# Kernel optimization log

Hardware: AMD Instinct MI355X
Metric: run time of the kernel (lower is better)

The kernel has to match this reference:

```python
import jax, jax.numpy as jnp
import numpy as np

B, QT, KT = 4, 1024, 1024
Q_SIZE, K_SIZE, EMB, HEADS = 1024, 1024, 1024, 8
HEAD_DIM = EMB // HEADS


def setup_inputs() -> dict:
    key = jax.random.key(0)
    ks = jax.random.split(key, 8)
    query = jax.random.normal(ks[0], (B, QT, Q_SIZE), dtype=jnp.float32)
    key_t = jax.random.normal(ks[1], (B, KT, K_SIZE), dtype=jnp.float32)
    mask = jax.random.randint(ks[2], (B, QT, KT), 0, 2, dtype=jnp.int32)
    # Linear weights stored as (in, out); torch Linear computes x @ W.T, equivalent here.
    sq = 1.0 / np.sqrt(Q_SIZE)
    sk = 1.0 / np.sqrt(K_SIZE)
    se = 1.0 / np.sqrt(EMB)
    Wq = jax.random.uniform(ks[3], (Q_SIZE, EMB), jnp.float32, -sq, sq)
    Wk = jax.random.uniform(ks[4], (K_SIZE, EMB), jnp.float32, -sk, sk)
    Wv = jax.random.uniform(ks[5], (K_SIZE, EMB), jnp.float32, -sk, sk)
    Wu = jax.random.uniform(ks[6], (EMB, EMB), jnp.float32, -se, se)
    bu = jax.random.uniform(ks[7], (EMB,), jnp.float32, -se, se)
    return {"query": query, "key": key_t, "mask": mask,
            "Wq": Wq, "Wk": Wk, "Wv": Wv, "Wu": Wu, "bu": bu}


def reference(query, key, mask, Wq, Wk, Wv, Wu, bu):
    b, q_t, _ = query.shape
    k_t = key.shape[1]
    q = (query @ Wq).reshape(b, q_t, HEADS, HEAD_DIM)   # b i n d
    k = (key @ Wk).reshape(b, k_t, HEADS, HEAD_DIM)     # b j n d
    v = (key @ Wv).reshape(b, k_t, HEADS, HEAD_DIM)
    # NOTE: original module defines self.scale but never applies it.
    att_score = jnp.einsum('bind,bjnd->bijn', q, k)
    att_score = jnp.where(mask[..., None] == 0, jnp.float32(-1e9), att_score)
    att_prob = jax.nn.softmax(att_score, axis=2)        # softmax over key axis j
    att_vec = jnp.einsum('bijn,bjnd->bind', att_prob, v).reshape(b, q_t, EMB)
    return att_vec @ Wu + bu
```

## Files before the change

### kernel.cpp

```cpp
#include <hip/hip_runtime.h>
#include <hip/hip_bf16.h>


typedef __attribute__((ext_vector_type(8))) short bf16x8;
typedef __attribute__((ext_vector_type(4))) float f32x4;

static constexpr int BB = 4;
static constexpr int TT = 1024;
static constexpr int EE = 1024;
static constexpr int HH = 8;
static constexpr int DD = 128;

static __device__ __forceinline__ unsigned short f2b(float x) {
  union { float f; unsigned int u; } c; c.f = x;
  unsigned int r = c.u + 0x7fffu + ((c.u >> 16) & 1u);
  return (unsigned short)(r >> 16);
}

static __device__ __forceinline__ unsigned int cvtpk(float lo, float hi) {
  unsigned int r;
  asm("v_cvt_pk_bf16_f32 %0, %1, %2" : "=v"(r) : "v"(lo), "v"(hi));
  return r;
}

static __device__ __forceinline__ float exp2x(float x) {
  float r;
  asm("v_exp_f32 %0, %1" : "=v"(r) : "v"(x));
  return r;
}

static __device__ __forceinline__ void gload_lds16(const void* g, void* l) {
  __builtin_amdgcn_global_load_lds(
      (const __attribute__((address_space(1))) unsigned int*)g,
      (__attribute__((address_space(3))) unsigned int*)l, 16, 0, 0);
}

__global__ __launch_bounds__(256) void cvt_kernel(
    const float* __restrict__ qf, const float* __restrict__ kf,
    unsigned short* __restrict__ qb, unsigned short* __restrict__ kb) {
  int i = blockIdx.x * 256 + threadIdx.x;
  float4 a = ((const float4*)qf)[i];
  ushort4 oa; oa.x = f2b(a.x); oa.y = f2b(a.y); oa.z = f2b(a.z); oa.w = f2b(a.w);
  ((ushort4*)qb)[i] = oa;
  float4 b = ((const float4*)kf)[i];
  ushort4 ob; ob.x = f2b(b.x); ob.y = f2b(b.y); ob.z = f2b(b.z); ob.w = f2b(b.w);
  ((ushort4*)kb)[i] = ob;
}

struct WT4 { const float* src[4]; unsigned short* dst[4]; float scale[4]; };

__global__ __launch_bounds__(256) void wtrans_kernel(WT4 wt) {
  const float* src = wt.src[blockIdx.z];
  unsigned short* dst = wt.dst[blockIdx.z];
  const float sc = wt.scale[blockIdx.z];
  __shared__ float tile[32][33];
  int n0 = blockIdx.x * 32, k0 = blockIdx.y * 32;
  int tx = threadIdx.x, ty = threadIdx.y;
#pragma unroll
  for (int i = 0; i < 4; ++i)
    tile[ty + i * 8][tx] = src[(size_t)(k0 + ty + i * 8) * EE + n0 + tx];
  __syncthreads();
#pragma unroll
  for (int i = 0; i < 4; ++i)
    dst[(size_t)(n0 + ty + i * 8) * EE + k0 + tx] = f2b(tile[tx][ty + i * 8] * sc);
}

__global__ __launch_bounds__(256) void vtrans_kernel(
    const unsigned short* __restrict__ vp, unsigned short* __restrict__ vt) {
  int bh = blockIdx.z; int b = bh >> 3, h = bh & 7;
  int d0 = blockIdx.x * 32, kt0 = blockIdx.y * 32;
  __shared__ unsigned short tile[32][33];
  int tx = threadIdx.x, ty = threadIdx.y;
#pragma unroll
  for (int i = 0; i < 4; ++i)
    tile[ty + i * 8][tx] =
        vp[(size_t)(b * TT + kt0 + ty + i * 8) * EE + h * DD + d0 + tx];
  __syncthreads();
#pragma unroll
  for (int i = 0; i < 4; ++i)
    vt[(size_t)((b * HH + h) * DD + d0 + ty + i * 8) * TT + kt0 + tx] =
        tile[tx][ty + i * 8];
}

__global__ __launch_bounds__(256) void maskpack_kernel(
    const int* __restrict__ mask, unsigned long long* __restrict__ mbits) {
  int row = blockIdx.x * 4 + (threadIdx.x >> 6);
  int lane = threadIdx.x & 63;
  const int* mrow = mask + (size_t)row * TT;
  unsigned long long myw = 0;
#pragma unroll
  for (int jw = 0; jw < 16; ++jw) {
    unsigned long long bal = __ballot(mrow[jw * 64 + lane] != 0);
    if (lane == jw) myw = bal;
  }
  if (lane < 16) mbits[(size_t)row * 16 + lane] = myw;
}

static __device__ __forceinline__ void gemm_core(
    const unsigned short* __restrict__ A, const unsigned short* __restrict__ Bt,
    unsigned short* __restrict__ Cb) {
  constexpr int K = EE, N = EE;
  __shared__ __align__(16) unsigned short As[128 * 64];
  __shared__ __align__(16) unsigned short Bs[128 * 64];
  const int tid = threadIdx.x, lane = tid & 63, w = tid >> 6;
  const int wm = w >> 1, wn = w & 1;
  const int bm = blockIdx.x, bn = blockIdx.y;
  const int g4 = lane >> 4, l15 = lane & 15;

  f32x4 acc[4][4] = {};

  for (int kt = 0; kt < K / 64; ++kt) {
    const int k0 = kt * 64;
#pragma unroll
    for (int it = 0; it < 4; ++it) {
      int idx = it * 256 + tid;
      int r = idx >> 3, c = (idx & 7) ^ (r & 7);
      gload_lds16(A + (size_t)(bm * 128 + r) * K + k0 + c * 8, As + idx * 8);
      gload_lds16(Bt + (size_t)(bn * 128 + r) * K + k0 + c * 8, Bs + idx * 8);
    }
    __syncthreads();
    bf16x8 af[2][4], bf[2][4];
#pragma unroll
    for (int kc2 = 0; kc2 < 2; ++kc2) {
      int co = ((kc2 * 4 + g4) ^ (l15 & 7)) * 8;
#pragma unroll
      for (int i = 0; i < 4; ++i) {
        af[kc2][i] = *(const bf16x8*)(As + (wm * 64 + i * 16 + l15) * 64 + co);
        bf[kc2][i] = *(const bf16x8*)(Bs + (wn * 64 + i * 16 + l15) * 64 + co);
      }
    }
#pragma unroll
    for (int kc2 = 0; kc2 < 2; ++kc2)
#pragma unroll
      for (int i = 0; i < 4; ++i)
#pragma unroll
        for (int j = 0; j < 4; ++j)
          acc[i][j] = __builtin_amdgcn_mfma_f32_16x16x32_bf16(
              af[kc2][i], bf[kc2][j], acc[i][j], 0, 0, 0);
    __syncthreads();
  }

  const int rr = g4 * 4;
#pragma unroll
  for (int i = 0; i < 4; ++i)
#pragma unroll
    for (int j = 0; j < 4; ++j) {
      int row = bm * 128 + wm * 64 + i * 16 + rr;
      int col = bn * 128 + wn * 64 + j * 16 + l15;
#pragma unroll
      for (int r = 0; r < 4; ++r)
        Cb[(size_t)(row + r) * N + col] = f2b(acc[i][j][r]);
    }
}

struct Gemm3 { const unsigned short* A[3]; const unsigned short* Bt[3];
               unsigned short* C[3]; };

__global__ __launch_bounds__(256) void proj_gemm_kernel(Gemm3 g) {
  int z = blockIdx.z;
  gemm_core(g.A[z], g.Bt[z], g.C[z]);
}

__global__ __launch_bounds__(256) void out_gemm_kernel(
    const unsigned short* __restrict__ A, const unsigned short* __restrict__ Bt,
    float* __restrict__ Cf, const float* __restrict__ bias) {
  constexpr int K = EE, N = EE;
  __shared__ __align__(16) unsigned short As[64 * 32];
  __shared__ __align__(16) unsigned short Bs[128 * 32];
  const int tid = threadIdx.x, lane = tid & 63, w = tid >> 6;
  const int wm = w >> 1, wn = w & 1;
  const int bm = blockIdx.x, bn = blockIdx.y;
  const int g4 = lane >> 4, l15 = lane & 15;

  f32x4 acc[2][4] = {};

  for (int kt = 0; kt < K / 32; ++kt) {
    const int k0 = kt * 32;
    {
      int row = tid >> 2, c = tid & 3;
      gload_lds16(A + (size_t)(bm * 64 + row) * K + k0 + c * 8, As + tid * 8);
    }
#pragma unroll
    for (int it = 0; it < 2; ++it) {
      int idx = it * 256 + tid;
      int row = idx >> 2, c = idx & 3;
      gload_lds16(Bt + (size_t)(bn * 128 + row) * K + k0 + c * 8, Bs + idx * 8);
    }
    __syncthreads();
    bf16x8 af[2], bf[4];
#pragma unroll
    for (int i = 0; i < 2; ++i)
      af[i] = *(const bf16x8*)(As + (wm * 32 + i * 16 + l15) * 32 + g4 * 8);
#pragma unroll
    for (int j = 0; j < 4; ++j)
      bf[j] = *(const bf16x8*)(Bs + (wn * 64 + j * 16 + l15) * 32 + g4 * 8);
#pragma unroll
    for (int i = 0; i < 2; ++i)
#pragma unroll
      for (int j = 0; j < 4; ++j)
        acc[i][j] = __builtin_amdgcn_mfma_f32_16x16x32_bf16(af[i], bf[j],
                                                            acc[i][j], 0, 0, 0);
    __syncthreads();
  }

  const int rr = g4 * 4;
#pragma unroll
  for (int i = 0; i < 2; ++i)
#pragma unroll
    for (int j = 0; j < 4; ++j) {
      int row = bm * 64 + wm * 32 + i * 16 + rr;
      int col = bn * 128 + wn * 64 + j * 16 + l15;
#pragma unroll
      for (int r = 0; r < 4; ++r)
        Cf[(size_t)(row + r) * N + col] = acc[i][j][r] + bias[col];
    }
}

__global__ __launch_bounds__(512, 4) void attn_kernel(
    const unsigned short* __restrict__ q, const unsigned short* __restrict__ k,
    const unsigned short* __restrict__ vt,
    const unsigned long long* __restrict__ mbits,
    unsigned short* __restrict__ av) {
  extern __shared__ __align__(16) char smem[];

  const int tid = threadIdx.x, lane = tid & 63, w = tid >> 6;
  const int grp = w >> 2, qw = w & 3;
  const int orig = blockIdx.x + 16 * blockIdx.y + 128 * blockIdx.z;
  const int qt = (orig >> 3) & 15;
  const int pair = ((orig & 7) << 2) | (orig >> 7);
  const int h = pair & 7, b = pair >> 3;
  const int i0 = qt * 64 + qw * 16;
  const int g4 = lane >> 4, l15 = lane & 15;
  const int swz = (l15 & 7) << 4;

  bf16x8 aq[4];
  {
    const unsigned short* qb =
        q + (size_t)(b * TT + i0 + l15) * EE + h * DD + g4 * 8;
#pragma unroll
    for (int kc = 0; kc < 4; ++kc) aq[kc] = *(const bf16x8*)(qb + kc * 32);
  }

  const unsigned short* sptr[4];
  int ldsb[4];
  size_t sadv;
  if (w < 4) {
    int kg = w >> 1, kh = w & 1;
    const unsigned short* kb0 = k + (size_t)(b * TT) * EE + h * DD;
#pragma unroll
    for (int p = 0; p < 4; ++p) {
      int idx = kh * 256 + p * 64 + lane;
      int kr = idx >> 4, c = (idx & 15) ^ (kr & 7);
      sptr[p] = kb0 + (size_t)(kg * 512 + kr) * EE + c * 8;
      ldsb[p] = kg * 8192 + (kh * 256 + p * 64) * 16;
    }
    sadv = (size_t)32 * EE;
  } else {
    int vw = w - 4;
    const unsigned short* vb0 = vt + (size_t)((b * HH + h) * DD) * TT;
#pragma unroll
    for (int p = 0; p < 4; ++p) {
      int cid = vw * 256 + p * 64 + lane;
      int d = cid >> 3, slot = cid & 7, eff = slot ^ (d & 7);
      sptr[p] = vb0 + (size_t)d * TT + (eff >> 2) * 512 + (eff & 3) * 8;
      ldsb[p] = 32768 + (vw * 256 + p * 64) * 16;
    }
    sadv = 32;
  }

  const unsigned* mb32 =
      (const unsigned*)mbits + ((size_t)(b * TT + i0 + l15) << 5) + grp * 16;
  unsigned mcur = mb32[0];

  int kb_[4];
#pragma unroll
  for (int kc = 0; kc < 4; ++kc)
    kb_[kc] = grp * 8192 + l15 * 256 + ((kc * 64 + g4 * 16) ^ swz);
  const int vb_ = 32768 + l15 * 128 + (((grp * 4 + g4) ^ (l15 & 7)) << 4);

#pragma unroll
  for (int p = 0; p < 4; ++p) gload_lds16(sptr[p], smem + ldsb[p]);
#pragma unroll
  for (int p = 0; p < 4; ++p) sptr[p] += sadv;

  f32x4 oacc[8] = {};
  float mrun = -__builtin_inff(), lrun = 0.f;

  __syncthreads();
  int bufoff = 0;

  for (int t = 0; t < 16; ++t) {
    unsigned mnext = 0;
    if (t < 15) {
      mnext = mb32[t + 1];
      int dst = bufoff ^ 16384;
#pragma unroll
      for (int p = 0; p < 4; ++p) gload_lds16(sptr[p], smem + dst + ldsb[p]);
#pragma unroll
      for (int p = 0; p < 4; ++p) sptr[p] += sadv;
    }

    f32x4 sacc[2] = {};
    __builtin_amdgcn_s_setprio(1);
#pragma unroll
    for (int kc = 0; kc < 4; ++kc)
#pragma unroll
      for (int nt = 0; nt < 2; ++nt) {
        bf16x8 bk = *(const bf16x8*)(smem + bufoff + kb_[kc] + nt * 4096);
        sacc[nt] = __builtin_amdgcn_mfma_f32_16x16x32_bf16(bk, aq[kc],
                                                           sacc[nt], 0, 0, 0);
      }
    __builtin_amdgcn_s_setprio(0);

#pragma unroll
    for (int nt = 0; nt < 2; ++nt)
#pragma unroll
      for (int r = 0; r < 4; ++r)
        if (((mcur >> (nt * 16 + g4 * 4 + r)) & 1u) == 0u)
          sacc[nt][r] = -1e9f;

    float mx = sacc[0][0];
#pragma unroll
    for (int nt = 0; nt < 2; ++nt)
#pragma unroll
      for (int r = 0; r < 4; ++r) mx = fmaxf(mx, sacc[nt][r]);
    mx = fmaxf(mx, __shfl_xor(mx, 16, 64));
    mx = fmaxf(mx, __shfl_xor(mx, 32, 64));

    if (__any(mx > mrun + 8.f)) {
      float mnew = fmaxf(mrun, mx);
      float sc = exp2x(mrun - mnew);
      lrun *= sc;
      mrun = mnew;
      float scO[4];
#pragma unroll
      for (int r = 0; r < 4; ++r)
        scO[r] = __shfl(sc, (lane & 48) | (((lane & 48) >> 2) + r), 64);
#pragma unroll
      for (int dt = 0; dt < 8; ++dt)
#pragma unroll
        for (int r = 0; r < 4; ++r) oacc[dt][r] *= scO[r];
    }

    float p2[2][4];
    float s0 = 0.f;
#pragma unroll
    for (int nt = 0; nt < 2; ++nt)
#pragma unroll
      for (int r = 0; r < 4; ++r) {
        float pv = exp2x(sacc[nt][r] - mrun);
        p2[nt][r] = pv;
        s0 += pv;
      }
    s0 += __shfl_xor(s0, 16, 64);
    s0 += __shfl_xor(s0, 32, 64);
    lrun += s0;

    unsigned int paw[4];
    {
      unsigned int D0a = cvtpk(p2[0][0], p2[0][1]);
      unsigned int D1a = cvtpk(p2[0][2], p2[0][3]);
      unsigned int D0b = cvtpk(p2[1][0], p2[1][1]);
      unsigned int D1b = cvtpk(p2[1][2], p2[1][3]);
      unsigned int r1 = __shfl_xor(g4 < 2 ? D0a : D0b, 16, 64);
      unsigned int r2 = __shfl_xor(g4 < 2 ? D1a : D1b, 16, 64);
      unsigned int r3 = __shfl_xor(g4 == 0 ? D0b : D0a, 32, 64);
      unsigned int r4 = __shfl_xor(g4 == 0 ? D1b : D1a, 32, 64);
      unsigned int r5 = __shfl_xor(g4 == 2 ? D0a : D0b, 48, 64);
      unsigned int r6 = __shfl_xor(g4 == 2 ? D1a : D1b, 48, 64);
      paw[0] = g4 == 0 ? D0a : g4 == 1 ? r5 : g4 == 2 ? r3 : r1;
      paw[1] = g4 == 0 ? D1a : g4 == 1 ? r6 : g4 == 2 ? r4 : r2;
      paw[2] = g4 == 0 ? r1 : g4 == 1 ? r3 : g4 == 2 ? r5 : D0b;
      paw[3] = g4 == 0 ? r2 : g4 == 1 ? r4 : g4 == 2 ? r6 : D1b;
    }

    __builtin_amdgcn_s_setprio(1);
    {
      union { unsigned int u[4]; bf16x8 v; } pau;
      pau.u[0] = paw[0]; pau.u[1] = paw[1];
      pau.u[2] = paw[2]; pau.u[3] = paw[3];
#pragma unroll
      for (int dt = 0; dt < 8; ++dt) {
        bf16x8 bv = *(const bf16x8*)(smem + bufoff + vb_ + dt * 2048);
        oacc[dt] = __builtin_amdgcn_mfma_f32_16x16x32_bf16(pau.v, bv, oacc[dt],
                                                           0, 0, 0);
      }
    }
    __builtin_amdgcn_s_setprio(0);

    __syncthreads();
    bufoff ^= 16384;
    mcur = mnext;
  }

  if (grp == 1) {
    char* ob = smem + qw * 8192 + lane * 128;
#pragma unroll
    for (int dt = 0; dt < 8; ++dt)
      *(f32x4*)(ob + ((dt ^ (lane & 7)) * 16)) = oacc[dt];
    float* mlb = (float*)(smem + 32768 + qw * 512 + lane * 8);
    mlb[0] = mrun; mlb[1] = lrun;
  }
  __syncthreads();
  if (grp == 0) {
    const char* ob = smem + qw * 8192 + lane * 128;
    const float* mlb = (const float*)(smem + 32768 + qw * 512 + lane * 8);
    float m2 = mlb[0], l2 = mlb[1];
    float ms = fmaxf(mrun, m2);
    float a1 = exp2x(mrun - ms), a2 = exp2x(m2 - ms);
    float lt = lrun * a1 + l2 * a2;
    float a1O[4], a2O[4], linv[4];
#pragma unroll
    for (int r = 0; r < 4; ++r) {
      int src = (lane & 48) | (((lane & 48) >> 2) + r);
      a1O[r] = __shfl(a1, src, 64);
      a2O[r] = __shfl(a2, src, 64);
      linv[r] = 1.f / __shfl(lt, src, 64);
    }
    unsigned short* obp =
        av + (size_t)(b * TT + i0 + g4 * 4) * EE + h * DD + l15;
#pragma unroll
    for (int dt = 0; dt < 8; ++dt) {
      f32x4 o2 = *(const f32x4*)(ob + ((dt ^ (lane & 7)) * 16));
#pragma unroll
      for (int r = 0; r < 4; ++r)
        obp[(size_t)r * EE + dt * 16] =
            f2b((oacc[dt][r] * a1O[r] + o2[r] * a2O[r]) * linv[r]);
    }
  }
}

extern "C" void kernel_launch(void* const* d_in, const int* in_sizes, int n_in,
                              void* d_out, int out_size, void* d_ws,
                              size_t ws_size, hipStream_t stream) {
  const float* query = (const float*)d_in[0];
  const float* key   = (const float*)d_in[1];
  const int*   mask  = (const int*)d_in[2];
  const float* Wq    = (const float*)d_in[3];
  const float* Wk    = (const float*)d_in[4];
  const float* Wv    = (const float*)d_in[5];
  const float* Wu    = (const float*)d_in[6];
  const float* bu    = (const float*)d_in[7];
  float* out = (float*)d_out;

  char* ws = (char*)d_ws;
  const size_t MB = 1024 * 1024;
  unsigned short* qbf = (unsigned short*)(ws);
  unsigned short* kbf = (unsigned short*)(ws + 8 * MB);
  unsigned short* Wqt = (unsigned short*)(ws + 16 * MB);
  unsigned short* Wkt = (unsigned short*)(ws + 18 * MB);
  unsigned short* Wvt = (unsigned short*)(ws + 20 * MB);
  unsigned short* Wut = (unsigned short*)(ws + 22 * MB);
  unsigned short* qp  = (unsigned short*)(ws + 24 * MB);
  unsigned short* kp  = (unsigned short*)(ws + 32 * MB);
  unsigned short* vp  = (unsigned short*)(ws + 40 * MB);
  unsigned short* vtb = (unsigned short*)(ws + 48 * MB);
  unsigned short* av  = (unsigned short*)(ws + 56 * MB);
  unsigned long long* mbt = (unsigned long long*)(ws + 40 * MB);

  cvt_kernel<<<4096, 256, 0, stream>>>(query, key, qbf, kbf);

  WT4 wt; wt.src[0] = Wq; wt.src[1] = Wk; wt.src[2] = Wv; wt.src[3] = Wu;
  wt.dst[0] = Wqt; wt.dst[1] = Wkt; wt.dst[2] = Wvt; wt.dst[3] = Wut;
  wt.scale[0] = 1.4426950408889634f;
  wt.scale[1] = 1.0f; wt.scale[2] = 1.0f; wt.scale[3] = 1.0f;
  wtrans_kernel<<<dim3(32, 32, 4), dim3(32, 8), 0, stream>>>(wt);

  Gemm3 g3;
  g3.A[0] = qbf; g3.A[1] = kbf; g3.A[2] = kbf;
  g3.Bt[0] = Wqt; g3.Bt[1] = Wkt; g3.Bt[2] = Wvt;
  g3.C[0] = qp; g3.C[1] = kp; g3.C[2] = vp;
  proj_gemm_kernel<<<dim3(32, 8, 3), 256, 0, stream>>>(g3);

  vtrans_kernel<<<dim3(4, 32, 32), dim3(32, 8), 0, stream>>>(vp, vtb);

  maskpack_kernel<<<1024, 256, 0, stream>>>(mask, mbt);

  attn_kernel<<<dim3(16, 8, 4), 512, 65536, stream>>>(qp, kp, vtb, mbt, av);

  out_gemm_kernel<<<dim3(64, 8), 256, 0, stream>>>(av, Wut, out, bu);
}
```

Before: 115.1 us.

## Merge prep and vtrans/maskpack launches; deepen out-GEMM K tile with swizzled LDS

Four small preprocessing kernels become two. The bf16 conversion and the weight transpose now share one launch, and the V transpose and mask bit-packing share another, with the work chosen by block index. The output GEMM now steps through K in chunks of 64 instead of 32, using XOR-swizzled LDS columns to avoid bank conflicts, which halves the number of loop iterations and barriers. The packed mask buffer moves to the q-bf16 workspace region, because its old location overlapped vp, which is now read in the same launch.

After: 107.2 us. 6.8% less time.

```diff
diff --git a/kernel.cpp b/kernel.cpp
--- a/kernel.cpp
+++ b/kernel.cpp
@@ -35,65 +35,75 @@
       (__attribute__((address_space(3))) unsigned int*)l, 16, 0, 0);
 }
 
-__global__ __launch_bounds__(256) void cvt_kernel(
-    const float* __restrict__ qf, const float* __restrict__ kf,
-    unsigned short* __restrict__ qb, unsigned short* __restrict__ kb) {
-  int i = blockIdx.x * 256 + threadIdx.x;
-  float4 a = ((const float4*)qf)[i];
-  ushort4 oa; oa.x = f2b(a.x); oa.y = f2b(a.y); oa.z = f2b(a.z); oa.w = f2b(a.w);
-  ((ushort4*)qb)[i] = oa;
-  float4 b = ((const float4*)kf)[i];
-  ushort4 ob; ob.x = f2b(b.x); ob.y = f2b(b.y); ob.z = f2b(b.z); ob.w = f2b(b.w);
-  ((ushort4*)kb)[i] = ob;
-}
-
-struct WT4 { const float* src[4]; unsigned short* dst[4]; float scale[4]; };
-
-__global__ __launch_bounds__(256) void wtrans_kernel(WT4 wt) {
-  const float* src = wt.src[blockIdx.z];
-  unsigned short* dst = wt.dst[blockIdx.z];
-  const float sc = wt.scale[blockIdx.z];
+struct PrepArgs {
+  const float* qf; const float* kf;
+  unsigned short* qb; unsigned short* kb;
+  const float* wsrc[4]; unsigned short* wdst[4]; float wscale[4];
+};
+
+__global__ __launch_bounds__(256) void prep_kernel(PrepArgs a) {
   __shared__ float tile[32][33];
-  int n0 = blockIdx.x * 32, k0 = blockIdx.y * 32;
-  int tx = threadIdx.x, ty = threadIdx.y;
-#pragma unroll
-  for (int i = 0; i < 4; ++i)
-    tile[ty + i * 8][tx] = src[(size_t)(k0 + ty + i * 8) * EE + n0 + tx];
-  __syncthreads();
-#pragma unroll
-  for (int i = 0; i < 4; ++i)
-    dst[(size_t)(n0 + ty + i * 8) * EE + k0 + tx] = f2b(tile[tx][ty + i * 8] * sc);
-}
-
-__global__ __launch_bounds__(256) void vtrans_kernel(
-    const unsigned short* __restrict__ vp, unsigned short* __restrict__ vt) {
-  int bh = blockIdx.z; int b = bh >> 3, h = bh & 7;
-  int d0 = blockIdx.x * 32, kt0 = blockIdx.y * 32;
+  const int bid = blockIdx.x, tid = threadIdx.x;
+  if (bid < 4096) {
+    int i = bid * 256 + tid;
+    float4 va = ((const float4*)a.qf)[i];
+    ushort4 oa; oa.x = f2b(va.x); oa.y = f2b(va.y);
+    oa.z = f2b(va.z); oa.w = f2b(va.w);
+    ((ushort4*)a.qb)[i] = oa;
+    float4 vb = ((const float4*)a.kf)[i];
+    ushort4 ob; ob.x = f2b(vb.x); ob.y = f2b(vb.y);
+    ob.z = f2b(vb.z); ob.w = f2b(vb.w);
+    ((ushort4*)a.kb)[i] = ob;
+  } else {
+    int g = bid - 4096;
+    int wz = g >> 10, rem = g & 1023;
+    int n0 = (rem & 31) * 32, k0 = (rem >> 5) * 32;
+    const float* src = a.wsrc[wz];
+    unsigned short* dst = a.wdst[wz];
+    const float sc = a.wscale[wz];
+    int tx = tid & 31, ty = tid >> 5;
+#pragma unroll
+    for (int i = 0; i < 4; ++i)
+      tile[ty + i * 8][tx] = src[(size_t)(k0 + ty + i * 8) * EE + n0 + tx];
+    __syncthreads();
+#pragma unroll
+    for (int i = 0; i < 4; ++i)
+      dst[(size_t)(n0 + ty + i * 8) * EE + k0 + tx] =
+          f2b(tile[tx][ty + i * 8] * sc);
+  }
+}
+
+__global__ __launch_bounds__(256) void vtrans_mask_kernel(
+    const unsigned short* __restrict__ vp, unsigned short* __restrict__ vt,
+    const int* __restrict__ mask, unsigned long long* __restrict__ mbits) {
   __shared__ unsigned short tile[32][33];
-  int tx = threadIdx.x, ty = threadIdx.y;
-#pragma unroll
-  for (int i = 0; i < 4; ++i)
-    tile[ty + i * 8][tx] =
-        vp[(size_t)(b * TT + kt0 + ty + i * 8) * EE + h * DD + d0 + tx];
-  __syncthreads();
-#pragma unroll
-  for (int i = 0; i < 4; ++i)
-    vt[(size_t)((b * HH + h) * DD + d0 + ty + i * 8) * TT + kt0 + tx] =
-        tile[tx][ty + i * 8];
-}
-
-__global__ __launch_bounds__(256) void maskpack_kernel(
-    const int* __restrict__ mask, unsigned long long* __restrict__ mbits) {
-  int row = blockIdx.x * 4 + (threadIdx.x >> 6);
-  int lane = threadIdx.x & 63;
-  const int* mrow = mask + (size_t)row * TT;
-  unsigned long long myw = 0;
-#pragma unroll
-  for (int jw = 0; jw < 16; ++jw) {
-    unsigned long long bal = __ballot(mrow[jw * 64 + lane] != 0);
-    if (lane == jw) myw = bal;
-  }
-  if (lane < 16) mbits[(size_t)row * 16 + lane] = myw;
+  const int bid = blockIdx.x, tid = threadIdx.x;
+  if (bid < 4096) {
+    int x = bid & 3, y = (bid >> 2) & 31, z = bid >> 7;
+    int b = z >> 3, h = z & 7;
+    int d0 = x * 32, kt0 = y * 32;
+    int tx = tid & 31, ty = tid >> 5;
+#pragma unroll
+    for (int i = 0; i < 4; ++i)
+      tile[ty + i * 8][tx] =
+          vp[(size_t)(b * TT + kt0 + ty + i * 8) * EE + h * DD + d0 + tx];
+    __syncthreads();
+#pragma unroll
+    for (int i = 0; i < 4; ++i)
+      vt[(size_t)((b * HH + h) * DD + d0 + ty + i * 8) * TT + kt0 + tx] =
+          tile[tx][ty + i * 8];
+  } else {
+    int row = (bid - 4096) * 4 + (tid >> 6);
+    int lane = tid & 63;
+    const int* mrow = mask + (size_t)row * TT;
+    unsigned long long myw = 0;
+#pragma unroll
+    for (int jw = 0; jw < 16; ++jw) {
+      unsigned long long bal = __ballot(mrow[jw * 64 + lane] != 0);
+      if (lane == jw) myw = bal;
+    }
+    if (lane < 16) mbits[(size_t)row * 16 + lane] = myw;
+  }
 }
 
 static __device__ __forceinline__ void gemm_core(
@@ -165,8 +175,8 @@
     const unsigned short* __restrict__ A, const unsigned short* __restrict__ Bt,
     float* __restrict__ Cf, const float* __restrict__ bias) {
   constexpr int K = EE, N = EE;
-  __shared__ __align__(16) unsigned short As[64 * 32];
-  __shared__ __align__(16) unsigned short Bs[128 * 32];
+  __shared__ __align__(16) unsigned short As[64 * 64];
+  __shared__ __align__(16) unsigned short Bs[128 * 64];
   const int tid = threadIdx.x, lane = tid & 63, w = tid >> 6;
   const int wm = w >> 1, wn = w & 1;
   const int bm = blockIdx.x, bn = blockIdx.y;
@@ -174,32 +184,40 @@
 
   f32x4 acc[2][4] = {};
 
-  for (int kt = 0; kt < K / 32; ++kt) {
-    const int k0 = kt * 32;
-    {
-      int row = tid >> 2, c = tid & 3;
-      gload_lds16(A + (size_t)(bm * 64 + row) * K + k0 + c * 8, As + tid * 8);
-    }
+  for (int kt = 0; kt < K / 64; ++kt) {
+    const int k0 = kt * 64;
 #pragma unroll
     for (int it = 0; it < 2; ++it) {
       int idx = it * 256 + tid;
-      int row = idx >> 2, c = idx & 3;
-      gload_lds16(Bt + (size_t)(bn * 128 + row) * K + k0 + c * 8, Bs + idx * 8);
-    }
-    __syncthreads();
-    bf16x8 af[2], bf[4];
-#pragma unroll
-    for (int i = 0; i < 2; ++i)
-      af[i] = *(const bf16x8*)(As + (wm * 32 + i * 16 + l15) * 32 + g4 * 8);
-#pragma unroll
-    for (int j = 0; j < 4; ++j)
-      bf[j] = *(const bf16x8*)(Bs + (wn * 64 + j * 16 + l15) * 32 + g4 * 8);
-#pragma unroll
-    for (int i = 0; i < 2; ++i)
+      int r = idx >> 3, c = (idx & 7) ^ (r & 7);
+      gload_lds16(A + (size_t)(bm * 64 + r) * K + k0 + c * 8, As + idx * 8);
+    }
+#pragma unroll
+    for (int it = 0; it < 4; ++it) {
+      int idx = it * 256 + tid;
+      int r = idx >> 3, c = (idx & 7) ^ (r & 7);
+      gload_lds16(Bt + (size_t)(bn * 128 + r) * K + k0 + c * 8, Bs + idx * 8);
+    }
+    __syncthreads();
+    bf16x8 af[2][2], bf[2][4];
+#pragma unroll
+    for (int kc2 = 0; kc2 < 2; ++kc2) {
+      int co = ((kc2 * 4 + g4) ^ (l15 & 7)) * 8;
+#pragma unroll
+      for (int i = 0; i < 2; ++i)
+        af[kc2][i] = *(const bf16x8*)(As + (wm * 32 + i * 16 + l15) * 64 + co);
 #pragma unroll
       for (int j = 0; j < 4; ++j)
-        acc[i][j] = __builtin_amdgcn_mfma_f32_16x16x32_bf16(af[i], bf[j],
-                                                            acc[i][j], 0, 0, 0);
+        bf[kc2][j] = *(const bf16x8*)(Bs + (wn * 64 + j * 16 + l15) * 64 + co);
+    }
+#pragma unroll
+    for (int kc2 = 0; kc2 < 2; ++kc2)
+#pragma unroll
+      for (int i = 0; i < 2; ++i)
+#pragma unroll
+        for (int j = 0; j < 4; ++j)
+          acc[i][j] = __builtin_amdgcn_mfma_f32_16x16x32_bf16(
+              af[kc2][i], bf[kc2][j], acc[i][j], 0, 0, 0);
     __syncthreads();
   }
 
@@ -456,15 +474,15 @@
   unsigned short* vp  = (unsigned short*)(ws + 40 * MB);
   unsigned short* vtb = (unsigned short*)(ws + 48 * MB);
   unsigned short* av  = (unsigned short*)(ws + 56 * MB);
-  unsigned long long* mbt = (unsigned long long*)(ws + 40 * MB);
-
-  cvt_kernel<<<4096, 256, 0, stream>>>(query, key, qbf, kbf);
-
-  WT4 wt; wt.src[0] = Wq; wt.src[1] = Wk; wt.src[2] = Wv; wt.src[3] = Wu;
-  wt.dst[0] = Wqt; wt.dst[1] = Wkt; wt.dst[2] = Wvt; wt.dst[3] = Wut;
-  wt.scale[0] = 1.4426950408889634f;
-  wt.scale[1] = 1.0f; wt.scale[2] = 1.0f; wt.scale[3] = 1.0f;
-  wtrans_kernel<<<dim3(32, 32, 4), dim3(32, 8), 0, stream>>>(wt);
+  unsigned long long* mbt = (unsigned long long*)(ws);
+
+  PrepArgs pa;
+  pa.qf = query; pa.kf = key; pa.qb = qbf; pa.kb = kbf;
+  pa.wsrc[0] = Wq; pa.wsrc[1] = Wk; pa.wsrc[2] = Wv; pa.wsrc[3] = Wu;
+  pa.wdst[0] = Wqt; pa.wdst[1] = Wkt; pa.wdst[2] = Wvt; pa.wdst[3] = Wut;
+  pa.wscale[0] = 1.4426950408889634f;
+  pa.wscale[1] = 1.0f; pa.wscale[2] = 1.0f; pa.wscale[3] = 1.0f;
+  prep_kernel<<<8192, 256, 0, stream>>>(pa);
 
   Gemm3 g3;
   g3.A[0] = qbf; g3.A[1] = kbf; g3.A[2] = kbf;
@@ -472,9 +490,7 @@
   g3.C[0] = qp; g3.C[1] = kp; g3.C[2] = vp;
   proj_gemm_kernel<<<dim3(32, 8, 3), 256, 0, stream>>>(g3);
 
-  vtrans_kernel<<<dim3(4, 32, 32), dim3(32, 8), 0, stream>>>(vp, vtb);
-
-  maskpack_kernel<<<1024, 256, 0, stream>>>(mask, mbt);
+  vtrans_mask_kernel<<<5120, 256, 0, stream>>>(vp, vtb, mask, mbt);
 
   attn_kernel<<<dim3(16, 8, 4), 512, 65536, stream>>>(qp, kp, vtb, mbt, av);
 
```
